# Performance work log

Measured on AMD Instinct MI355X. Metric: run time of the kernel, lower is better.

Reference implementation:

```python
import jax, jax.numpy as jnp
import numpy as np

NUM_HEADS = 8
BN_EPS = 1e-5


def setup_inputs() -> dict:
    key = jax.random.key(0)
    ks = jax.random.split(key, 7)
    B, C, T, N = 16, 512, 128, 64
    x = jax.random.normal(ks[0], (B, C, T, N), dtype=jnp.float32)
    # 1x1 convs stored as [out, in] matrices
    w_qkv = jax.random.normal(ks[1], (3 * C, C), dtype=jnp.float32) * (1.0 / np.sqrt(C))
    b_qkv = jax.random.normal(ks[2], (3 * C,), dtype=jnp.float32) * 0.01
    w_proj = jax.random.normal(ks[3], (C, C), dtype=jnp.float32) * (1.0 / np.sqrt(C))
    b_proj = jax.random.normal(ks[4], (C,), dtype=jnp.float32) * 0.01
    gamma = jnp.ones((C,), dtype=jnp.float32) + 0.1 * jax.random.normal(ks[5], (C,), dtype=jnp.float32)
    beta = 0.1 * jax.random.normal(ks[6], (C,), dtype=jnp.float32)
    return {"x": x, "w_qkv": w_qkv, "b_qkv": b_qkv, "w_proj": w_proj,
            "b_proj": b_proj, "gamma": gamma, "beta": beta}


def reference(x, w_qkv, b_qkv, w_proj, b_proj, gamma, beta):
    B, C, T, N = x.shape
    H = NUM_HEADS
    hd = C // H
    scale = 1.0 / np.sqrt(hd).astype(np.float32)

    # qkv 1x1 conv: [B,3C,T,N]
    qkv = jnp.einsum('bctn,oc->botn', x, w_qkv) + b_qkv[None, :, None, None]
    q, k, v = jnp.split(qkv, 3, axis=1)

    def to_heads(t):  # [B,C,T,N] -> [B,H,T,N,hd]
        return t.reshape(B, H, hd, T, N).transpose(0, 1, 3, 4, 2)

    q, k, v = to_heads(q), to_heads(k), to_heads(v)

    # unnormalized attention over the N (node) axis, no softmax
    attn = jnp.einsum('bhtnd,bhtmd->bhtnm', q, k) * scale  # [B,H,T,N,N]
    out = jnp.einsum('bhtnm,bhtmd->bhtnd', attn, v)        # [B,H,T,N,hd]

    # back to [B,C,T,N]
    out = out.transpose(0, 1, 4, 2, 3).reshape(B, C, T, N)

    # proj 1x1 conv
    out = jnp.einsum('bctn,oc->botn', out, w_proj) + b_proj[None, :, None, None]

    # BatchNorm2d (training-mode batch statistics, biased variance, eps=1e-5)
    mean = out.mean(axis=(0, 2, 3))
    var = out.var(axis=(0, 2, 3))
    out = (out - mean[None, :, None, None]) * (gamma / jnp.sqrt(var + BN_EPS))[None, :, None, None] \
          + beta[None, :, None, None]

    return out + x
```

## Files before the change

kernel.cpp:

```cpp
#include <hip/hip_runtime.h>

typedef unsigned int uint;
typedef unsigned short ushort;
typedef short short8 __attribute__((ext_vector_type(8)));
typedef float floatx4 __attribute__((ext_vector_type(4)));
typedef ushort ushortx8 __attribute__((ext_vector_type(8)));
typedef ushort ushortx4 __attribute__((ext_vector_type(4)));
typedef uint uintx4 __attribute__((ext_vector_type(4)));

#define DEV static __device__ __forceinline__

#define Bsz 16
#define Cch 512
#define Tt 128
#define Nn 64
#define Hh 8
#define HD 64
#define Pp 8192
#define BPOS 131072
#define C3 1536

DEV int swz(int row, int c8) { return row * 8 + (c8 ^ (row & 7) ^ ((row >> 3) & 7)); }

DEV ushort f2bf(float f) {
  uint u = __float_as_uint(f);
  return (ushort)((u + 0x7FFFu + ((u >> 16) & 1u)) >> 16);
}
DEV float bf2f(ushort h) { return __uint_as_float(((uint)h) << 16); }

DEV void gll16(const ushort* src, ushort* dst) {
  __builtin_amdgcn_global_load_lds(
      (const __attribute__((address_space(1))) unsigned int*)src,
      (__attribute__((address_space(3))) unsigned int*)dst, 16, 0, 0);
}

__global__ __launch_bounds__(256) void k_cvt(const float* __restrict__ src,
                                             ushort* __restrict__ dst, int n) {
  int gid = blockIdx.x * 256 + threadIdx.x;
  int i8 = gid * 8;
  if (i8 < n) {
    floatx4 a = *(const floatx4*)&src[i8];
    floatx4 b = *(const floatx4*)&src[i8 + 4];
    ushortx8 o;
#pragma unroll
    for (int j = 0; j < 4; ++j) { o[j] = f2bf(a[j]); o[j + 4] = f2bf(b[j]); }
    *(ushortx8*)&dst[i8] = o;
  }
}

__global__ __launch_bounds__(256) void k_transpose_x(const float* __restrict__ x,
                                                     ushort* __restrict__ xT) {
  int p0 = blockIdx.x * 64, c0 = blockIdx.y * 64, b = blockIdx.z;
  __shared__ __align__(16) ushort sm[4096];
  int tid = threadIdx.x;
  const float* xb = x + (size_t)b * Cch * Pp;
  ushort* xTb = xT + (size_t)b * Pp * Cch;
#pragma unroll
  for (int it = 0; it < 4; ++it) {
    int cc = tid + it * 256;
    int r = cc >> 4, c4 = cc & 15;
    floatx4 v = *(const floatx4*)&xb[(size_t)(c0 + r) * Pp + p0 + c4 * 4];
    ushortx4 o;
#pragma unroll
    for (int j = 0; j < 4; ++j) o[j] = f2bf(v[j]);
    *(ushortx4*)&sm[swz(r, c4 >> 1) * 8 + (c4 & 1) * 4] = o;
  }
  __syncthreads();
#pragma unroll
  for (int it = 0; it < 2; ++it) {
    int cc = tid + it * 256;
    int pl = cc >> 3, c8 = cc & 7;
    ushortx8 o;
#pragma unroll
    for (int j = 0; j < 8; ++j) {
      int c = c8 * 8 + j;
      o[j] = sm[swz(c, pl >> 3) * 8 + (pl & 7)];
    }
    *(ushortx8*)&xTb[(size_t)(p0 + pl) * Cch + c0 + c8 * 8] = o;
  }
}

__global__ __launch_bounds__(256) void k_gemm_bt(const ushort* __restrict__ A,
                                                 const ushort* __restrict__ W,
                                                 const float* __restrict__ bias,
                                                 ushort* __restrict__ D,
                                                 int K, int ldD,
                                                 size_t sAb, size_t sDb) {
  __shared__ __align__(16) ushort sm[32768];
  int tid = threadIdx.x;
  int lane = tid & 63, w = tid >> 6;
  int wm = (w & 1) * 64, wn = (w >> 1) * 64;
  size_t m0 = (size_t)blockIdx.y * 128;
  size_t n0 = (size_t)blockIdx.x * 128;
  const ushort* Ab = A + (size_t)blockIdx.z * sAb;
  ushort* Db = D + (size_t)blockIdx.z * sDb;

  const ushort *aS[4], *wS[4];
#pragma unroll
  for (int it = 0; it < 4; ++it) {
    int i = it * 256 + tid;
    int r = i >> 3;
    int c8 = (i & 7) ^ (r & 7) ^ ((r >> 3) & 7);
    aS[it] = &Ab[(m0 + r) * (size_t)K + c8 * 8];
    wS[it] = &W[(n0 + r) * (size_t)K + c8 * 8];
  }
  int dof = w * 512;

  floatx4 zero4 = {0.f, 0.f, 0.f, 0.f};
  floatx4 acc[4][4];
#pragma unroll
  for (int i = 0; i < 4; ++i)
#pragma unroll
    for (int j = 0; j < 4; ++j) acc[i][j] = zero4;

  const int NT = K >> 6;
#pragma unroll
  for (int it = 0; it < 4; ++it) {
    gll16(aS[it], &sm[it * 2048 + dof]);
    gll16(wS[it], &sm[8192 + it * 2048 + dof]);
  }
  __syncthreads();

  int cur = 0;
  for (int t = 0; t < NT; ++t) {
    ushort* cA = sm + (cur << 14);
    ushort* cB = cA + 8192;
    if (t + 1 < NT) {
      ushort* nA = sm + ((cur ^ 1) << 14);
      ushort* nB = nA + 8192;
      int kb = (t + 1) << 6;
#pragma unroll
      for (int it = 0; it < 4; ++it) {
        gll16(aS[it] + kb, &nA[it * 2048 + dof]);
        gll16(wS[it] + kb, &nB[it * 2048 + dof]);
      }
    }
#pragma unroll
    for (int kk = 0; kk < 2; ++kk) {
      int g = kk * 4 + (lane >> 4);
      int rr = lane & 15;
      short8 af[4], bf[4];
#pragma unroll
      for (int i = 0; i < 4; ++i) af[i] = *(const short8*)&cA[swz(wm + i * 16 + rr, g) * 8];
#pragma unroll
      for (int j = 0; j < 4; ++j) bf[j] = *(const short8*)&cB[swz(wn + j * 16 + rr, g) * 8];
#pragma unroll
      for (int i = 0; i < 4; ++i)
#pragma unroll
        for (int j = 0; j < 4; ++j)
          acc[i][j] = __builtin_amdgcn_mfma_f32_16x16x32_bf16(af[i], bf[j], acc[i][j], 0, 0, 0);
    }
    __syncthreads();
    cur ^= 1;
  }

  int quad = lane >> 4, col = lane & 15;
#pragma unroll
  for (int j = 0; j < 4; ++j) {
    int n_loc = wn + j * 16 + col;
    float bj = bias[n0 + n_loc];
#pragma unroll
    for (int i = 0; i < 4; ++i)
#pragma unroll
      for (int r = 0; r < 4; ++r) {
        int m_loc = wm + i * 16 + quad * 4 + r;
        sm[(m_loc * 16 + ((n_loc >> 3) ^ (m_loc & 7) ^ ((m_loc >> 3) & 7))) * 8 + (n_loc & 7)] =
            f2bf(acc[i][j][r] + bj);
      }
  }
  __syncthreads();
#pragma unroll
  for (int it = 0; it < 8; ++it) {
    int cc = tid + it * 256;
    int m_loc = cc >> 4, cn = cc & 15;
    uintx4 v = *(const uintx4*)&sm[(m_loc * 16 + (cn ^ (m_loc & 7) ^ ((m_loc >> 3) & 7))) * 8];
    *(uintx4*)&Db[(m0 + m_loc) * (size_t)ldD + n0 + cn * 8] = v;
  }
}

__global__ __launch_bounds__(256) void k_gemm2_t(const ushort* __restrict__ A,
                                                 const ushort* __restrict__ W,
                                                 const float* __restrict__ bias,
                                                 float* __restrict__ D,
                                                 int K, int ldD,
                                                 size_t sAb, size_t sDb, int bBase,
                                                 float* __restrict__ psum,
                                                 float* __restrict__ psq) {
  __shared__ __align__(16) ushort sm[32768];
  float* smf = (float*)sm;
  int tid = threadIdx.x;
  int lane = tid & 63, w = tid >> 6;
  int wm = (w & 1) * 64, wn = (w >> 1) * 64;
  size_t m0 = (size_t)blockIdx.y * 128;
  size_t n0 = (size_t)blockIdx.x * 128;
  const ushort* Ab = A + (size_t)blockIdx.z * sAb;
  float* Db = D + (size_t)blockIdx.z * sDb;
  int part = (bBase + blockIdx.z) * 64 + blockIdx.y;

  const ushort *aS[4], *wS[4];
#pragma unroll
  for (int it = 0; it < 4; ++it) {
    int i = it * 256 + tid;
    int r = i >> 3;
    int c8 = (i & 7) ^ (r & 7) ^ ((r >> 3) & 7);
    aS[it] = &Ab[(m0 + r) * (size_t)K + c8 * 8];
    wS[it] = &W[(n0 + r) * (size_t)K + c8 * 8];
  }
  int dof = w * 512;

  floatx4 zero4 = {0.f, 0.f, 0.f, 0.f};
  floatx4 acc[4][4];
#pragma unroll
  for (int i = 0; i < 4; ++i)
#pragma unroll
    for (int j = 0; j < 4; ++j) acc[i][j] = zero4;

  const int NT = K >> 6;
#pragma unroll
  for (int it = 0; it < 4; ++it) {
    gll16(aS[it], &sm[it * 2048 + dof]);
    gll16(wS[it], &sm[8192 + it * 2048 + dof]);
  }
  __syncthreads();

  int cur = 0;
  for (int t = 0; t < NT; ++t) {
    ushort* cA = sm + (cur << 14);
    ushort* cB = cA + 8192;
    if (t + 1 < NT) {
      ushort* nA = sm + ((cur ^ 1) << 14);
      ushort* nB = nA + 8192;
      int kb = (t + 1) << 6;
#pragma unroll
      for (int it = 0; it < 4; ++it) {
        gll16(aS[it] + kb, &nA[it * 2048 + dof]);
        gll16(wS[it] + kb, &nB[it * 2048 + dof]);
      }
    }
#pragma unroll
    for (int kk = 0; kk < 2; ++kk) {
      int g = kk * 4 + (lane >> 4);
      int rr = lane & 15;
      short8 af[4], bf[4];
#pragma unroll
      for (int i = 0; i < 4; ++i) af[i] = *(const short8*)&cA[swz(wm + i * 16 + rr, g) * 8];
#pragma unroll
      for (int j = 0; j < 4; ++j) bf[j] = *(const short8*)&cB[swz(wn + j * 16 + rr, g) * 8];
#pragma unroll
      for (int i = 0; i < 4; ++i)
#pragma unroll
        for (int j = 0; j < 4; ++j)
          acc[i][j] = __builtin_amdgcn_mfma_f32_16x16x32_bf16(af[i], bf[j], acc[i][j], 0, 0, 0);
    }
    __syncthreads();
    cur ^= 1;
  }

  int quad = lane >> 4, col = lane & 15;
#pragma unroll
  for (int h = 0; h < 2; ++h) {
    __syncthreads();
    if ((w >> 1) == h) {
#pragma unroll
      for (int j = 0; j < 4; ++j) {
        int n1 = j * 16 + col;
        float bj = bias[n0 + h * 64 + n1];
#pragma unroll
        for (int i = 0; i < 4; ++i) {
          int mb = wm + i * 16 + quad * 4;
          floatx4 v4;
#pragma unroll
          for (int r = 0; r < 4; ++r) v4[r] = acc[i][j][r] + bj;
          *(floatx4*)&smf[n1 * 128 + (mb ^ ((n1 & 7) << 2))] = v4;
        }
      }
    }
    __syncthreads();
#pragma unroll
    for (int it = 0; it < 8; ++it) {
      int cc = tid + it * 256;
      int n2 = cc >> 5, ck = cc & 31;
      floatx4 v = *(const floatx4*)&smf[n2 * 128 + ((ck * 4) ^ ((n2 & 7) << 2))];
      *(floatx4*)&Db[(n0 + h * 64 + n2) * (size_t)ldD + m0 + ck * 4] = v;
      float s = v[0] + v[1] + v[2] + v[3];
      float q = v[0] * v[0] + v[1] * v[1] + v[2] * v[2] + v[3] * v[3];
#pragma unroll
      for (int off = 16; off > 0; off >>= 1) {
        s += __shfl_down(s, off, 32);
        q += __shfl_down(q, off, 32);
      }
      if ((tid & 31) == 0) {
        size_t c = n0 + h * 64 + n2;
        psum[c * 1024 + part] = s;
        psq[c * 1024 + part] = q;
      }
    }
  }
}

__global__ __launch_bounds__(256) void k_attn(const ushort* __restrict__ qkv,
                                              ushort* __restrict__ aT,
                                              size_t sQb, size_t sAb) {
  int bx = blockIdx.x;
  int t = bx & 127, h = bx >> 7;
  __shared__ __align__(16) ushort sm[16384];
  ushort* qs = sm;
  ushort* ks = sm + 4096;
  ushort* vt = sm + 8192;
  ushort* ss = sm + 12288;
  int tid = threadIdx.x, lane = tid & 63, w = tid >> 6;
  int quad = lane >> 4, col = lane & 15;
  const ushort* base = qkv + (size_t)blockIdx.y * sQb + (size_t)(t * 64) * C3 + h * 64;

#pragma unroll
  for (int it = 0; it < 2; ++it) {
    int i = it * 256 + tid;
    int r = i >> 3;
    int c8 = (i & 7) ^ (r & 7) ^ ((r >> 3) & 7);
    gll16(&base[(size_t)r * C3 + c8 * 8], &qs[(size_t)(it * 256 + w * 64) * 8]);
    gll16(&base[(size_t)r * C3 + 512 + c8 * 8], &ks[(size_t)(it * 256 + w * 64) * 8]);
    int n = i >> 3, d8 = i & 7;
    ushortx8 vv = *(const ushortx8*)&base[(size_t)n * C3 + 1024 + d8 * 8];
#pragma unroll
    for (int j = 0; j < 8; ++j) {
      int dp = d8 * 8 + j;
      vt[swz(dp, n >> 3) * 8 + (n & 7)] = vv[j];
    }
  }
  __syncthreads();

  floatx4 zero4 = {0.f, 0.f, 0.f, 0.f};
  floatx4 accs[4] = {zero4, zero4, zero4, zero4};
#pragma unroll
  for (int kk = 0; kk < 2; ++kk) {
    int g = kk * 4 + quad;
    short8 aq = *(const short8*)&qs[swz(w * 16 + col, g) * 8];
#pragma unroll
    for (int j = 0; j < 4; ++j) {
      short8 bk = *(const short8*)&ks[swz(j * 16 + col, g) * 8];
      accs[j] = __builtin_amdgcn_mfma_f32_16x16x32_bf16(aq, bk, accs[j], 0, 0, 0);
    }
  }
#pragma unroll
  for (int j = 0; j < 4; ++j)
#pragma unroll
    for (int r = 0; r < 4; ++r) {
      int n = w * 16 + quad * 4 + r, m = j * 16 + col;
      ss[swz(n, m >> 3) * 8 + (m & 7)] = f2bf(accs[j][r] * 0.125f);
    }
  __syncthreads();

  floatx4 acco[4] = {zero4, zero4, zero4, zero4};
#pragma unroll
  for (int kk = 0; kk < 2; ++kk) {
    int g = kk * 4 + quad;
    short8 as = *(const short8*)&ss[swz(w * 16 + col, g) * 8];
#pragma unroll
    for (int j = 0; j < 4; ++j) {
      short8 bv = *(const short8*)&vt[swz(j * 16 + col, g) * 8];
      acco[j] = __builtin_amdgcn_mfma_f32_16x16x32_bf16(as, bv, acco[j], 0, 0, 0);
    }
  }
#pragma unroll
  for (int j = 0; j < 4; ++j)
#pragma unroll
    for (int r = 0; r < 4; ++r) {
      int n = w * 16 + quad * 4 + r, dp = j * 16 + col;
      qs[swz(n, dp >> 3) * 8 + (dp & 7)] = f2bf(acco[j][r]);
    }
  __syncthreads();
  ushort* aTb = aT + (size_t)blockIdx.y * sAb + (size_t)(t * 64) * Cch + h * 64;
#pragma unroll
  for (int it = 0; it < 2; ++it) {
    int cc = tid + it * 256;
    int n = cc >> 3, c8 = cc & 7;
    uintx4 v = *(const uintx4*)&qs[swz(n, c8) * 8];
    *(uintx4*)&aTb[(size_t)n * Cch + c8 * 8] = v;
  }
}

__global__ __launch_bounds__(256) void k_bnfin(const float* __restrict__ psum,
                                               const float* __restrict__ psq,
                                               const float* __restrict__ gamma,
                                               const float* __restrict__ beta,
                                               float* __restrict__ scaleS,
                                               float* __restrict__ shiftS) {
  int c = blockIdx.x;
  int tid = threadIdx.x;
  floatx4 v = *(const floatx4*)&psum[(size_t)c * 1024 + tid * 4];
  floatx4 u = *(const floatx4*)&psq[(size_t)c * 1024 + tid * 4];
  float s = v[0] + v[1] + v[2] + v[3];
  float q = u[0] + u[1] + u[2] + u[3];
#pragma unroll
  for (int off = 32; off > 0; off >>= 1) {
    s += __shfl_down(s, off);
    q += __shfl_down(q, off);
  }
  __shared__ float rs[4], rq[4];
  if ((tid & 63) == 0) { rs[tid >> 6] = s; rq[tid >> 6] = q; }
  __syncthreads();
  if (tid == 0) {
    float S = rs[0] + rs[1] + rs[2] + rs[3];
    float Q = rq[0] + rq[1] + rq[2] + rq[3];
    float inv = 1.0f / (float)BPOS;
    float mean = S * inv;
    float var = Q * inv - mean * mean;
    float sc = gamma[c] * rsqrtf(var + 1e-5f);
    scaleS[c] = sc;
    shiftS[c] = beta[c] - mean * sc;
  }
}

__global__ __launch_bounds__(256) void k_final(const float* __restrict__ x,
                                               float* __restrict__ y,
                                               const float* __restrict__ scaleS,
                                               const float* __restrict__ shiftS) {
  size_t gid = (size_t)blockIdx.x * 256 + threadIdx.x;
  size_t i4 = gid * 4;
  int c = (int)((i4 >> 13) & 511);
  float sc = scaleS[c], sh = shiftS[c];
  floatx4 yv = *(floatx4*)&y[i4];
  floatx4 xv = *(const floatx4*)&x[i4];
  floatx4 o;
#pragma unroll
  for (int j = 0; j < 4; ++j) o[j] = yv[j] * sc + sh + xv[j];
  *(floatx4*)&y[i4] = o;
}

extern "C" void kernel_launch(void* const* d_in, const int* in_sizes, int n_in,
                              void* d_out, int out_size, void* d_ws, size_t ws_size,
                              hipStream_t stream) {
  const float* x      = (const float*)d_in[0];
  const float* w_qkv  = (const float*)d_in[1];
  const float* b_qkv  = (const float*)d_in[2];
  const float* w_proj = (const float*)d_in[3];
  const float* b_proj = (const float*)d_in[4];
  const float* gamma  = (const float*)d_in[5];
  const float* beta   = (const float*)d_in[6];
  float* outf = (float*)d_out;

  char* ws = (char*)d_ws;
  ushort* qkv_ws = (ushort*)ws;
  float*  psum   = (float*)ws;
  float*  psq    = (float*)(ws + 2097152ull);
  ushort* aT_ws  = (ushort*)(ws + 25165824ull);
  ushort* wqkvb  = (ushort*)(ws + 33554432ull);
  ushort* wprojb = (ushort*)(ws + 35127296ull);
  float*  st     = (float*)(ws + 35651584ull);
  float* scaleS = st, *shiftS = st + 512;

  ushort* xT   = (ushort*)((char*)d_out + 134217728ull);
  ushort* qkvL = (ushort*)d_out;

  const size_t PC = (size_t)Pp * Cch;
  const size_t PQ = (size_t)Pp * C3;
  const size_t CP = (size_t)Cch * Pp;

  k_cvt<<<dim3(384), 256, 0, stream>>>(w_qkv, wqkvb, 3 * Cch * Cch);
  k_cvt<<<dim3(128), 256, 0, stream>>>(w_proj, wprojb, Cch * Cch);
  k_transpose_x<<<dim3(Pp / 64, Cch / 64, Bsz), 256, 0, stream>>>(x, xT);

  for (int g = 0; g < 3; ++g) {
    int b0 = g * 5;
    k_gemm_bt<<<dim3(C3 / 128, Pp / 128, 5), 256, 0, stream>>>(
        xT + (size_t)b0 * PC, wqkvb, b_qkv, qkvL, Cch, C3, PC, PQ);
    k_attn<<<dim3(Hh * Tt, 5), 256, 0, stream>>>(qkvL, xT + (size_t)b0 * PC, PQ, PC);
  }
  k_gemm_bt<<<dim3(C3 / 128, Pp / 128, 1), 256, 0, stream>>>(
      xT + 15 * PC, wqkvb, b_qkv, qkv_ws, Cch, C3, 0, 0);
  k_attn<<<dim3(Hh * Tt, 1), 256, 0, stream>>>(qkv_ws, aT_ws, 0, 0);

  k_gemm2_t<<<dim3(Cch / 128, Pp / 128, 8), 256, 0, stream>>>(
      xT + 0 * PC, wprojb, b_proj, outf + 0 * CP, Cch, Pp, PC, CP, 0, psum, psq);
  k_gemm2_t<<<dim3(Cch / 128, Pp / 128, 4), 256, 0, stream>>>(
      xT + 8 * PC, wprojb, b_proj, outf + 8 * CP, Cch, Pp, PC, CP, 8, psum, psq);
  k_gemm2_t<<<dim3(Cch / 128, Pp / 128, 2), 256, 0, stream>>>(
      xT + 12 * PC, wprojb, b_proj, outf + 12 * CP, Cch, Pp, PC, CP, 12, psum, psq);
  k_gemm2_t<<<dim3(Cch / 128, Pp / 128, 1), 256, 0, stream>>>(
      xT + 14 * PC, wprojb, b_proj, outf + 14 * CP, Cch, Pp, 0, 0, 14, psum, psq);
  k_gemm2_t<<<dim3(Cch / 128, Pp / 128, 1), 256, 0, stream>>>(
      aT_ws, wprojb, b_proj, outf + 15 * CP, Cch, Pp, 0, 0, 15, psum, psq);

  k_bnfin<<<dim3(Cch), 256, 0, stream>>>(psum, psq, gamma, beta, scaleS, shiftS);
  k_final<<<dim3(BPOS * Cch / 4 / 256), 256, 0, stream>>>(x, outf, scaleS, shiftS);
}
```

Measured before the change: 1.201 ms.

## Store projection output as bf16 and merge proj GEMM launches into one

The projection GEMM now writes its pre-BatchNorm output as bf16 instead of fp32, and the BN statistics are computed from the rounded values. This lets all 16 batches run in a single launch, with batch 0 redirected to a workspace buffer to avoid aliasing. The final kernel reads bf16 y and writes fp32 output, processing batches in reverse order so it does not overwrite unread bf16 data sharing the output buffer. The aim is to cut the intermediate's memory traffic and launch count, at the cost of bf16 rounding in the pre-normalisation values and tighter buffer-aliasing logic.

```diff
diff --git a/kernel.cpp b/kernel.cpp
--- a/kernel.cpp
+++ b/kernel.cpp
@@ -181,9 +181,10 @@
 __global__ __launch_bounds__(256) void k_gemm2_t(const ushort* __restrict__ A,
                                                  const ushort* __restrict__ W,
                                                  const float* __restrict__ bias,
-                                                 float* __restrict__ D,
+                                                 ushort* __restrict__ yL,
+                                                 ushort* __restrict__ y0,
                                                  int K, int ldD,
-                                                 size_t sAb, size_t sDb, int bBase,
+                                                 size_t sAb, size_t sDb,
                                                  float* __restrict__ psum,
                                                  float* __restrict__ psq) {
   __shared__ __align__(16) ushort sm[32768];
@@ -194,8 +195,8 @@
   size_t m0 = (size_t)blockIdx.y * 128;
   size_t n0 = (size_t)blockIdx.x * 128;
   const ushort* Ab = A + (size_t)blockIdx.z * sAb;
-  float* Db = D + (size_t)blockIdx.z * sDb;
-  int part = (bBase + blockIdx.z) * 64 + blockIdx.y;
+  ushort* Db = (blockIdx.z == 0) ? y0 : yL + (size_t)blockIdx.z * sDb;
+  int part = blockIdx.z * 64 + blockIdx.y;
 
   const ushort *aS[4], *wS[4];
 #pragma unroll
@@ -281,9 +282,17 @@
       int cc = tid + it * 256;
       int n2 = cc >> 5, ck = cc & 31;
       floatx4 v = *(const floatx4*)&smf[n2 * 128 + ((ck * 4) ^ ((n2 & 7) << 2))];
-      *(floatx4*)&Db[(n0 + h * 64 + n2) * (size_t)ldD + m0 + ck * 4] = v;
-      float s = v[0] + v[1] + v[2] + v[3];
-      float q = v[0] * v[0] + v[1] * v[1] + v[2] * v[2] + v[3] * v[3];
+      ushortx4 o;
+#pragma unroll
+      for (int r = 0; r < 4; ++r) o[r] = f2bf(v[r]);
+      *(ushortx4*)&Db[(n0 + h * 64 + n2) * (size_t)ldD + m0 + ck * 4] = o;
+      float s = 0.f, q = 0.f;
+#pragma unroll
+      for (int r = 0; r < 4; ++r) {
+        float f = bf2f(o[r]);
+        s += f;
+        q += f * f;
+      }
 #pragma unroll
       for (int off = 16; off > 0; off >>= 1) {
         s += __shfl_down(s, off, 32);
@@ -412,19 +421,25 @@
 }
 
 __global__ __launch_bounds__(256) void k_final(const float* __restrict__ x,
-                                               float* __restrict__ y,
+                                               const ushort* __restrict__ y,
+                                               float* __restrict__ out,
                                                const float* __restrict__ scaleS,
                                                const float* __restrict__ shiftS) {
   size_t gid = (size_t)blockIdx.x * 256 + threadIdx.x;
-  size_t i4 = gid * 4;
-  int c = (int)((i4 >> 13) & 511);
+  size_t i8 = gid * 8;
+  int c = (int)((i8 >> 13) & 511);
   float sc = scaleS[c], sh = shiftS[c];
-  floatx4 yv = *(floatx4*)&y[i4];
-  floatx4 xv = *(const floatx4*)&x[i4];
-  floatx4 o;
-#pragma unroll
-  for (int j = 0; j < 4; ++j) o[j] = yv[j] * sc + sh + xv[j];
-  *(floatx4*)&y[i4] = o;
+  ushortx8 yv = *(const ushortx8*)&y[i8];
+  floatx4 x0 = *(const floatx4*)&x[i8];
+  floatx4 x1 = *(const floatx4*)&x[i8 + 4];
+  floatx4 o0, o1;
+#pragma unroll
+  for (int j = 0; j < 4; ++j) {
+    o0[j] = bf2f(yv[j]) * sc + sh + x0[j];
+    o1[j] = bf2f(yv[j + 4]) * sc + sh + x1[j];
+  }
+  *(floatx4*)&out[i8] = o0;
+  *(floatx4*)&out[i8 + 4] = o1;
 }
 
 extern "C" void kernel_launch(void* const* d_in, const int* in_sizes, int n_in,
@@ -440,10 +455,9 @@
   float* outf = (float*)d_out;
 
   char* ws = (char*)d_ws;
-  ushort* qkv_ws = (ushort*)ws;
   float*  psum   = (float*)ws;
   float*  psq    = (float*)(ws + 2097152ull);
-  ushort* aT_ws  = (ushort*)(ws + 25165824ull);
+  ushort* y0ws   = (ushort*)(ws + 4194304ull);
   ushort* wqkvb  = (ushort*)(ws + 33554432ull);
   ushort* wprojb = (ushort*)(ws + 35127296ull);
   float*  st     = (float*)(ws + 35651584ull);
@@ -451,6 +465,7 @@
 
   ushort* xT   = (ushort*)((char*)d_out + 134217728ull);
   ushort* qkvL = (ushort*)d_out;
+  ushort* yL   = (ushort*)d_out;
 
   const size_t PC = (size_t)Pp * Cch;
   const size_t PQ = (size_t)Pp * C3;
@@ -467,20 +482,17 @@
     k_attn<<<dim3(Hh * Tt, 5), 256, 0, stream>>>(qkvL, xT + (size_t)b0 * PC, PQ, PC);
   }
   k_gemm_bt<<<dim3(C3 / 128, Pp / 128, 1), 256, 0, stream>>>(
-      xT + 15 * PC, wqkvb, b_qkv, qkv_ws, Cch, C3, 0, 0);
-  k_attn<<<dim3(Hh * Tt, 1), 256, 0, stream>>>(qkv_ws, aT_ws, 0, 0);
-
-  k_gemm2_t<<<dim3(Cch / 128, Pp / 128, 8), 256, 0, stream>>>(
-      xT + 0 * PC, wprojb, b_proj, outf + 0 * CP, Cch, Pp, PC, CP, 0, psum, psq);
-  k_gemm2_t<<<dim3(Cch / 128, Pp / 128, 4), 256, 0, stream>>>(
-      xT + 8 * PC, wprojb, b_proj, outf + 8 * CP, Cch, Pp, PC, CP, 8, psum, psq);
-  k_gemm2_t<<<dim3(Cch / 128, Pp / 128, 2), 256, 0, stream>>>(
-      xT + 12 * PC, wprojb, b_proj, outf + 12 * CP, Cch, Pp, PC, CP, 12, psum, psq);
-  k_gemm2_t<<<dim3(Cch / 128, Pp / 128, 1), 256, 0, stream>>>(
-      xT + 14 * PC, wprojb, b_proj, outf + 14 * CP, Cch, Pp, 0, 0, 14, psum, psq);
-  k_gemm2_t<<<dim3(Cch / 128, Pp / 128, 1), 256, 0, stream>>>(
-      aT_ws, wprojb, b_proj, outf + 15 * CP, Cch, Pp, 0, 0, 15, psum, psq);
+      xT + 15 * PC, wqkvb, b_qkv, qkvL, Cch, C3, 0, 0);
+  k_attn<<<dim3(Hh * Tt, 1), 256, 0, stream>>>(qkvL, xT + 15 * PC, 0, 0);
+
+  k_gemm2_t<<<dim3(Cch / 128, Pp / 128, 16), 256, 0, stream>>>(
+      xT, wprojb, b_proj, yL, y0ws, Cch, Pp, PC, PC, psum, psq);
 
   k_bnfin<<<dim3(Cch), 256, 0, stream>>>(psum, psq, gamma, beta, scaleS, shiftS);
-  k_final<<<dim3(BPOS * Cch / 4 / 256), 256, 0, stream>>>(x, outf, scaleS, shiftS);
-}
+
+  k_final<<<dim3(8 * 2048), 256, 0, stream>>>(x + 8 * CP, yL + 8 * PC, outf + 8 * CP, scaleS, shiftS);
+  k_final<<<dim3(4 * 2048), 256, 0, stream>>>(x + 4 * CP, yL + 4 * PC, outf + 4 * CP, scaleS, shiftS);
+  k_final<<<dim3(2 * 2048), 256, 0, stream>>>(x + 2 * CP, yL + 2 * PC, outf + 2 * CP, scaleS, shiftS);
+  k_final<<<dim3(1 * 2048), 256, 0, stream>>>(x + 1 * CP, yL + 1 * PC, outf + 1 * CP, scaleS, shiftS);
+  k_final<<<dim3(1 * 2048), 256, 0, stream>>>(x, y0ws, outf, scaleS, shiftS);
+}
```

New measurement: 1.157 ms. 1.04x faster.
